# Optimization experiments

Measured on AMD Instinct MI355X. Metric: run time of the kernel, lower is better.

The kernel has to match this reference:

```python
import jax, jax.numpy as jnp
import numpy as np

N = 250000
E = 4000000
IN_F, HID, OUT = 18, 16, 1


def setup_inputs() -> dict:
    key = jax.random.key(0)
    ks = jax.random.split(key, 7)
    x = jax.random.normal(ks[0], (N, IN_F), dtype=jnp.float32)
    edge_index = jax.random.randint(ks[1], (2, E), 0, N, dtype=jnp.int64)
    # GCNConv params (PyG uses Glorot for weight, zeros for bias)
    W1 = jax.random.normal(ks[2], (IN_F, HID), dtype=jnp.float32) * (1.0 / np.sqrt(IN_F))
    b1 = jnp.zeros((HID,), dtype=jnp.float32)
    W2 = jax.random.normal(ks[3], (HID, OUT), dtype=jnp.float32) * (1.0 / np.sqrt(HID))
    b2 = jnp.zeros((OUT,), dtype=jnp.float32)
    return {"x": x, "edge_index": edge_index, "W1": W1, "b1": b1, "W2": W2, "b2": b2}


def _gcn_conv(x, W, b, src, dst, norm, n_nodes):
    # linear transform then degree-normalized scatter-add (PyG GCNConv)
    h = x @ W                                  # [N, F_out]
    msg = h[src] * norm[:, None]               # gather + per-edge scale
    out = jax.ops.segment_sum(msg, dst, num_segments=n_nodes)
    return out + b


def reference(x, edge_index, W1, b1, W2, b2):
    # add self-loops (GCNConv default add_self_loops=True)
    loops = jnp.arange(N, dtype=edge_index.dtype)
    src = jnp.concatenate([edge_index[0], loops])
    dst = jnp.concatenate([edge_index[1], loops])
    # symmetric normalization: deg computed at destination over self-looped graph
    deg = jax.ops.segment_sum(jnp.ones_like(dst, dtype=x.dtype), dst, num_segments=N)
    dis = jnp.where(deg > 0, jax.lax.rsqrt(deg), 0.0)
    norm = dis[src] * dis[dst]                 # [E+N]
    h = _gcn_conv(x, W1, b1, src, dst, norm, N)
    h = jax.nn.relu(h)
    # dropout is identity in eval mode (F.dropout(training=self.training))
    out = _gcn_conv(h, W2, b2, src, dst, norm, N)
    return out
```

## Files before the change

### kernel.cpp

```cpp
#include <hip/hip_runtime.h>
#include <hip/hip_fp16.h>


#define NB_BITS 8
#define BN (1 << NB_BITS)
#define SB_BITS 9
#define SBN (1 << SB_BITS)
#define NSB 512
#define BIN_TPB 512
#define BIN_CHUNK 8192
#define AGG_TPB 512

__device__ __forceinline__ int exscan512(int v, int* warpsums, int t) {
    int lane = t & 63, w = t >> 6;
    int x = v;
#pragma unroll
    for (int off = 1; off < 64; off <<= 1) {
        int y = __shfl_up(x, off);
        if (lane >= off) x += y;
    }
    if (lane == 63) warpsums[w] = x;
    __syncthreads();
    if (w == 0) {
        int s = (lane < 8) ? warpsums[lane] : 0;
#pragma unroll
        for (int off = 1; off < 8; off <<= 1) {
            int y = __shfl_up(s, off);
            if (lane >= off) s += y;
        }
        if (lane < 8) warpsums[lane] = s;
    }
    __syncthreads();
    int base = (w > 0) ? warpsums[w - 1] : 0;
    return base + x - v;
}

__global__ void bhist_kernel(const int* __restrict__ dst, int* __restrict__ bcnt, int E) {
    __shared__ int cnt[NSB];
    int t = threadIdx.x;
    cnt[t] = 0;
    __syncthreads();
    int base = blockIdx.x * BIN_CHUNK;
    int end = min(base + BIN_CHUNK, E);
    if (end - base == BIN_CHUNK) {
        const int4* d4 = (const int4*)(dst + base);
#pragma unroll
        for (int i = 0; i < BIN_CHUNK / (BIN_TPB * 4); i++) {
            int4 v = d4[t + i * BIN_TPB];
            atomicAdd(&cnt[v.x >> SB_BITS], 1);
            atomicAdd(&cnt[v.y >> SB_BITS], 1);
            atomicAdd(&cnt[v.z >> SB_BITS], 1);
            atomicAdd(&cnt[v.w >> SB_BITS], 1);
        }
    } else {
        for (int e = base + t; e < end; e += BIN_TPB)
            atomicAdd(&cnt[dst[e] >> SB_BITS], 1);
    }
    __syncthreads();
    if (cnt[t] > 0) atomicAdd(&bcnt[t], cnt[t]);
}

__global__ void bscan_kernel(const int* __restrict__ bcnt, int* __restrict__ bstart,
                             int* __restrict__ cursor) {
    __shared__ int warpsums[8];
    int t = threadIdx.x;
    int v = bcnt[t];
    int excl = exscan512(v, warpsums, t);
    bstart[t] = excl;
    cursor[t] = excl;
    if (t == NSB - 1) bstart[NSB] = excl + v;
}

__global__ void bplace_kernel(const int* __restrict__ src, const int* __restrict__ dst,
                              int* __restrict__ cursor, int* __restrict__ pairs, int E) {
    __shared__ int cnt[NSB];
    __shared__ int lstart[NSB];
    __shared__ int lcur[NSB];
    __shared__ int gbase[NSB];
    __shared__ int warpsums[8];
    __shared__ int lbuf[BIN_CHUNK];
    __shared__ unsigned short lbin[BIN_CHUNK];
    int t = threadIdx.x;
    int base = blockIdx.x * BIN_CHUNK;
    int end = min(base + BIN_CHUNK, E);
    int full = (end - base == BIN_CHUNK);
    cnt[t] = 0;
    __syncthreads();
    if (full) {
        const int4* d4 = (const int4*)(dst + base);
#pragma unroll
        for (int i = 0; i < BIN_CHUNK / (BIN_TPB * 4); i++) {
            int4 v = d4[t + i * BIN_TPB];
            atomicAdd(&cnt[v.x >> SB_BITS], 1);
            atomicAdd(&cnt[v.y >> SB_BITS], 1);
            atomicAdd(&cnt[v.z >> SB_BITS], 1);
            atomicAdd(&cnt[v.w >> SB_BITS], 1);
        }
    } else {
        for (int e = base + t; e < end; e += BIN_TPB)
            atomicAdd(&cnt[dst[e] >> SB_BITS], 1);
    }
    __syncthreads();
    int v = cnt[t];
    int excl = exscan512(v, warpsums, t);
    lstart[t] = excl;
    lcur[t] = excl;
    gbase[t] = (v > 0) ? atomicAdd(&cursor[t], v) : 0;
    __syncthreads();
    if (full) {
        const int4* s4 = (const int4*)(src + base);
        const int4* d4 = (const int4*)(dst + base);
#pragma unroll
        for (int i = 0; i < BIN_CHUNK / (BIN_TPB * 4); i++) {
            int4 dv = d4[t + i * BIN_TPB];
            int4 sv = s4[t + i * BIN_TPB];
            int b0 = dv.x >> SB_BITS, p0 = atomicAdd(&lcur[b0], 1);
            lbuf[p0] = (sv.x << SB_BITS) | (dv.x & (SBN - 1));
            lbin[p0] = (unsigned short)b0;
            int b1 = dv.y >> SB_BITS, p1 = atomicAdd(&lcur[b1], 1);
            lbuf[p1] = (sv.y << SB_BITS) | (dv.y & (SBN - 1));
            lbin[p1] = (unsigned short)b1;
            int b2 = dv.z >> SB_BITS, p2 = atomicAdd(&lcur[b2], 1);
            lbuf[p2] = (sv.z << SB_BITS) | (dv.z & (SBN - 1));
            lbin[p2] = (unsigned short)b2;
            int b3 = dv.w >> SB_BITS, p3 = atomicAdd(&lcur[b3], 1);
            lbuf[p3] = (sv.w << SB_BITS) | (dv.w & (SBN - 1));
            lbin[p3] = (unsigned short)b3;
        }
    } else {
        for (int e = base + t; e < end; e += BIN_TPB) {
            int d = dst[e], s = src[e];
            int b = d >> SB_BITS;
            int pos = atomicAdd(&lcur[b], 1);
            lbuf[pos] = (s << SB_BITS) | (d & (SBN - 1));
            lbin[pos] = (unsigned short)b;
        }
    }
    __syncthreads();
    int n = end - base;
#pragma unroll 4
    for (int i = t; i < n; i += BIN_TPB) {
        int b = lbin[i];
        pairs[gbase[b] + (i - lstart[b])] = lbuf[i];
    }
}

__global__ void csr_kernel(const int* __restrict__ pairs, const int* __restrict__ bstart,
                           int* __restrict__ rowp, int* __restrict__ csr_src,
                           float* __restrict__ dis, const float* __restrict__ x,
                           const float* __restrict__ W1, __half* __restrict__ hs1h,
                           int N) {
    __shared__ int cnt[SBN];
    __shared__ int warpsums[8];
    __shared__ float w[18 * 16];
    int b = blockIdx.x, t = threadIdx.x;
    int s0 = bstart[b], s1 = bstart[b + 1];
    cnt[t] = 0;
    if (t < 18 * 16) w[t] = W1[t];
    __syncthreads();
#pragma unroll 4
    for (int e = s0 + t; e < s1; e += SBN)
        atomicAdd(&cnt[pairs[e] & (SBN - 1)], 1);
    __syncthreads();
    int v = cnt[t];
    int excl = exscan512(v, warpsums, t);
    int nbase = b << SB_BITS;
    int start = s0 + excl;
    rowp[nbase + t] = start;
    int n = nbase + t;
    float dv = rsqrtf((float)v + 1.0f);
    if (n < N) dis[n] = dv;
    __syncthreads();
    cnt[t] = start;
    if (t == 0) rowp[nbase + SBN] = s1;
    __syncthreads();
#pragma unroll 4
    for (int e = s0 + t; e < s1; e += SBN) {
        int pv = pairs[e];
        int pos = atomicAdd(&cnt[pv & (SBN - 1)], 1);
        csr_src[pos] = pv >> SB_BITS;
    }
    if (n < N) {
        const float2* x2 = (const float2*)(x + (size_t)n * 18);
        float xv[18];
#pragma unroll
        for (int k = 0; k < 9; k++) {
            float2 vv = x2[k];
            xv[2 * k] = vv.x;
            xv[2 * k + 1] = vv.y;
        }
        float acc[16];
#pragma unroll
        for (int f = 0; f < 16; f++) acc[f] = 0.0f;
#pragma unroll
        for (int k = 0; k < 18; k++) {
            float xk = xv[k];
#pragma unroll
            for (int f = 0; f < 16; f++) acc[f] = fmaf(xk, w[k * 16 + f], acc[f]);
        }
        unsigned int u[8];
#pragma unroll
        for (int q = 0; q < 8; q++) {
            unsigned int lo = __half_as_ushort(__float2half_rn(acc[2 * q] * dv));
            unsigned int hi = __half_as_ushort(__float2half_rn(acc[2 * q + 1] * dv));
            u[q] = lo | (hi << 16);
        }
        uint4* outp = (uint4*)(hs1h + (size_t)n * 16);
        outp[0] = make_uint4(u[0], u[1], u[2], u[3]);
        outp[1] = make_uint4(u[4], u[5], u[6], u[7]);
    }
}

__global__ void agg1_kernel(const int* __restrict__ csr_src, const int* __restrict__ rowp,
                            const __half* __restrict__ hs1h, const float* __restrict__ dis,
                            const float* __restrict__ b1, const float* __restrict__ W2,
                            float* __restrict__ hs2, int N) {
    int b = blockIdx.x, t = threadIdx.x;
    int f = t & 15;
    int g = t >> 4;
    float bbf = b1[f], wwf = W2[f];
    int nbase = b << NB_BITS;
    for (int nl = g; nl < BN; nl += AGG_TPB / 16) {
        int n = nbase + nl;
        if (n >= N) continue;
        int r0 = rowp[n], r1 = rowp[n + 1];
        float a = 0.f;
#pragma unroll 4
        for (int r = r0; r < r1; ++r) {
            int s = csr_src[r];
            a += __half2float(hs1h[(size_t)s * 16 + f]);
        }
        float d = dis[n];
        float self = __half2float(hs1h[(size_t)n * 16 + f]);
        float p = fmaxf(d * (a + self) + bbf, 0.f) * wwf;
        p += __shfl_xor(p, 1);
        p += __shfl_xor(p, 2);
        p += __shfl_xor(p, 4);
        p += __shfl_xor(p, 8);
        if (f == 0) hs2[n] = p * d;
    }
}

__global__ void agg2_kernel(const int* __restrict__ csr_src, const int* __restrict__ rowp,
                            const float* __restrict__ hs2, const float* __restrict__ dis,
                            const float* __restrict__ b2, float* __restrict__ out, int N) {
    int b = blockIdx.x, t = threadIdx.x;
    int l = t & 15;
    int g = t >> 4;
    int nbase = b << NB_BITS;
    float bb = b2[0];
    for (int nl = g; nl < BN; nl += AGG_TPB / 16) {
        int n = nbase + nl;
        if (n >= N) continue;
        int r0 = rowp[n], r1 = rowp[n + 1];
        float a = 0.f;
        for (int r = r0 + l; r < r1; r += 16) a += hs2[csr_src[r]];
        a += __shfl_xor(a, 1);
        a += __shfl_xor(a, 2);
        a += __shfl_xor(a, 4);
        a += __shfl_xor(a, 8);
        if (l == 0) out[n] = dis[n] * (a + hs2[n]) + bb;
    }
}

extern "C" void kernel_launch(void* const* d_in, const int* in_sizes, int n_in,
                              void* d_out, int out_size, void* d_ws, size_t ws_size,
                              hipStream_t stream) {
    const float* x = (const float*)d_in[0];
    const int* edge_index = (const int*)d_in[1];
    const float* W1 = (const float*)d_in[2];
    const float* b1 = (const float*)d_in[3];
    const float* W2 = (const float*)d_in[4];
    const float* b2 = (const float*)d_in[5];
    float* out = (float*)d_out;

    const int N = in_sizes[0] / 18;
    const int E = in_sizes[1] / 2;
    const int* src = edge_index;
    const int* dst = edge_index + E;
    const int NABUCKET = (N + BN - 1) / BN;
    const int NSBUCKET = (N + SBN - 1) / SBN;

    int* ws = (int*)d_ws;
    int* pairs = ws;
    int* csr_src = pairs + (size_t)E;
    __half* hs1h = (__half*)(csr_src + (size_t)E);
    float* hs2 = (float*)((int*)(csr_src + (size_t)E) + 8 * (size_t)N);
    float* dis = hs2 + N;
    int* rowp = (int*)(dis + N);
    int* bstart = rowp + (size_t)NSBUCKET * SBN + 1;
    int* cursor = bstart + NSB + 1;
    int* bcnt = cursor + NSB;

    hipMemsetAsync(bcnt, 0, NSB * sizeof(int), stream);

    int binBlocks = (E + BIN_CHUNK - 1) / BIN_CHUNK;

    bhist_kernel<<<binBlocks, BIN_TPB, 0, stream>>>(dst, bcnt, E);
    bscan_kernel<<<1, NSB, 0, stream>>>(bcnt, bstart, cursor);
    bplace_kernel<<<binBlocks, BIN_TPB, 0, stream>>>(src, dst, cursor, pairs, E);
    csr_kernel<<<NSBUCKET, SBN, 0, stream>>>(pairs, bstart, rowp, csr_src, dis,
                                             x, W1, hs1h, N);
    agg1_kernel<<<NABUCKET, AGG_TPB, 0, stream>>>(csr_src, rowp, hs1h, dis, b1, W2, hs2, N);
    agg2_kernel<<<NABUCKET, AGG_TPB, 0, stream>>>(csr_src, rowp, hs2, dis, b2, out, N);
}
```

Baseline: 246.7 us.

## Replace global bucket histogram pass with per-chunk sort and segmented CSR build

Drops the global histogram and scan kernels. Each chunk now sorts its edges locally into buckets and writes them contiguously, along with per-chunk bucket offsets. The CSR kernel gathers its bucket's segments from every chunk and claims its output region with an atomic allocator, so rows no longer come out in global order and rowp gains a per-bucket layout. The dis array is removed and the normalisation is recomputed from the row length inside the aggregation kernels. This saves two launches and one full read of dst. The cost is that in the CSR kernel each thread walks one chunk's segment serially, giving uncoalesced, imbalanced loads with only about 489 of 512 threads active.

```diff
diff --git a/kernel.cpp b/kernel.cpp
--- a/kernel.cpp
+++ b/kernel.cpp
@@ -35,14 +35,19 @@
     return base + x - v;
 }
 
-__global__ void bhist_kernel(const int* __restrict__ dst, int* __restrict__ bcnt, int E) {
+__global__ void sortchunk_kernel(const int* __restrict__ src, const int* __restrict__ dst,
+                                 int* __restrict__ pairs, int* __restrict__ pofs, int E) {
     __shared__ int cnt[NSB];
-    int t = threadIdx.x;
+    __shared__ int lcur[NSB];
+    __shared__ int warpsums[8];
+    __shared__ int lbuf[BIN_CHUNK];
+    int t = threadIdx.x, c = blockIdx.x;
+    int base = c * BIN_CHUNK;
+    int end = min(base + BIN_CHUNK, E);
+    int full = (end - base == BIN_CHUNK);
     cnt[t] = 0;
     __syncthreads();
-    int base = blockIdx.x * BIN_CHUNK;
-    int end = min(base + BIN_CHUNK, E);
-    if (end - base == BIN_CHUNK) {
+    if (full) {
         const int4* d4 = (const int4*)(dst + base);
 #pragma unroll
         for (int i = 0; i < BIN_CHUNK / (BIN_TPB * 4); i++) {
@@ -57,55 +62,11 @@
             atomicAdd(&cnt[dst[e] >> SB_BITS], 1);
     }
     __syncthreads();
-    if (cnt[t] > 0) atomicAdd(&bcnt[t], cnt[t]);
-}
-
-__global__ void bscan_kernel(const int* __restrict__ bcnt, int* __restrict__ bstart,
-                             int* __restrict__ cursor) {
-    __shared__ int warpsums[8];
-    int t = threadIdx.x;
-    int v = bcnt[t];
-    int excl = exscan512(v, warpsums, t);
-    bstart[t] = excl;
-    cursor[t] = excl;
-    if (t == NSB - 1) bstart[NSB] = excl + v;
-}
-
-__global__ void bplace_kernel(const int* __restrict__ src, const int* __restrict__ dst,
-                              int* __restrict__ cursor, int* __restrict__ pairs, int E) {
-    __shared__ int cnt[NSB];
-    __shared__ int lstart[NSB];
-    __shared__ int lcur[NSB];
-    __shared__ int gbase[NSB];
-    __shared__ int warpsums[8];
-    __shared__ int lbuf[BIN_CHUNK];
-    __shared__ unsigned short lbin[BIN_CHUNK];
-    int t = threadIdx.x;
-    int base = blockIdx.x * BIN_CHUNK;
-    int end = min(base + BIN_CHUNK, E);
-    int full = (end - base == BIN_CHUNK);
-    cnt[t] = 0;
-    __syncthreads();
-    if (full) {
-        const int4* d4 = (const int4*)(dst + base);
-#pragma unroll
-        for (int i = 0; i < BIN_CHUNK / (BIN_TPB * 4); i++) {
-            int4 v = d4[t + i * BIN_TPB];
-            atomicAdd(&cnt[v.x >> SB_BITS], 1);
-            atomicAdd(&cnt[v.y >> SB_BITS], 1);
-            atomicAdd(&cnt[v.z >> SB_BITS], 1);
-            atomicAdd(&cnt[v.w >> SB_BITS], 1);
-        }
-    } else {
-        for (int e = base + t; e < end; e += BIN_TPB)
-            atomicAdd(&cnt[dst[e] >> SB_BITS], 1);
-    }
-    __syncthreads();
     int v = cnt[t];
     int excl = exscan512(v, warpsums, t);
-    lstart[t] = excl;
     lcur[t] = excl;
-    gbase[t] = (v > 0) ? atomicAdd(&cursor[t], v) : 0;
+    pofs[(size_t)c * (NSB + 1) + t] = excl;
+    if (t == 0) pofs[(size_t)c * (NSB + 1) + NSB] = end - base;
     __syncthreads();
     if (full) {
         const int4* s4 = (const int4*)(src + base);
@@ -116,16 +77,12 @@
             int4 sv = s4[t + i * BIN_TPB];
             int b0 = dv.x >> SB_BITS, p0 = atomicAdd(&lcur[b0], 1);
             lbuf[p0] = (sv.x << SB_BITS) | (dv.x & (SBN - 1));
-            lbin[p0] = (unsigned short)b0;
             int b1 = dv.y >> SB_BITS, p1 = atomicAdd(&lcur[b1], 1);
             lbuf[p1] = (sv.y << SB_BITS) | (dv.y & (SBN - 1));
-            lbin[p1] = (unsigned short)b1;
             int b2 = dv.z >> SB_BITS, p2 = atomicAdd(&lcur[b2], 1);
             lbuf[p2] = (sv.z << SB_BITS) | (dv.z & (SBN - 1));
-            lbin[p2] = (unsigned short)b2;
             int b3 = dv.w >> SB_BITS, p3 = atomicAdd(&lcur[b3], 1);
             lbuf[p3] = (sv.w << SB_BITS) | (dv.w & (SBN - 1));
-            lbin[p3] = (unsigned short)b3;
         }
     } else {
         for (int e = base + t; e < end; e += BIN_TPB) {
@@ -133,50 +90,52 @@
             int b = d >> SB_BITS;
             int pos = atomicAdd(&lcur[b], 1);
             lbuf[pos] = (s << SB_BITS) | (d & (SBN - 1));
-            lbin[pos] = (unsigned short)b;
         }
     }
     __syncthreads();
     int n = end - base;
 #pragma unroll 4
-    for (int i = t; i < n; i += BIN_TPB) {
-        int b = lbin[i];
-        pairs[gbase[b] + (i - lstart[b])] = lbuf[i];
-    }
-}
-
-__global__ void csr_kernel(const int* __restrict__ pairs, const int* __restrict__ bstart,
-                           int* __restrict__ rowp, int* __restrict__ csr_src,
-                           float* __restrict__ dis, const float* __restrict__ x,
+    for (int i = t; i < n; i += BIN_TPB) pairs[base + i] = lbuf[i];
+}
+
+__global__ void csr_kernel(const int* __restrict__ pairs, const int* __restrict__ pofs,
+                           int* __restrict__ alloc, int* __restrict__ rowp,
+                           int* __restrict__ csr_src, const float* __restrict__ x,
                            const float* __restrict__ W1, __half* __restrict__ hs1h,
-                           int N) {
+                           int N, int NCHUNK) {
     __shared__ int cnt[SBN];
     __shared__ int warpsums[8];
     __shared__ float w[18 * 16];
+    __shared__ int regbase_s;
     int b = blockIdx.x, t = threadIdx.x;
-    int s0 = bstart[b], s1 = bstart[b + 1];
     cnt[t] = 0;
     if (t < 18 * 16) w[t] = W1[t];
-    __syncthreads();
-#pragma unroll 4
-    for (int e = s0 + t; e < s1; e += SBN)
-        atomicAdd(&cnt[pairs[e] & (SBN - 1)], 1);
+    int seg0 = 0, seg1 = 0;
+    if (t < NCHUNK) {
+        int s = pofs[(size_t)t * (NSB + 1) + b];
+        int e = pofs[(size_t)t * (NSB + 1) + b + 1];
+        seg0 = t * BIN_CHUNK + s;
+        seg1 = t * BIN_CHUNK + e;
+    }
+    __syncthreads();
+    for (int i = seg0; i < seg1; ++i)
+        atomicAdd(&cnt[pairs[i] & (SBN - 1)], 1);
     __syncthreads();
     int v = cnt[t];
     int excl = exscan512(v, warpsums, t);
+    if (t == 0) regbase_s = atomicAdd(alloc, warpsums[7]);
+    __syncthreads();
+    int regbase = regbase_s;
     int nbase = b << SB_BITS;
-    int start = s0 + excl;
-    rowp[nbase + t] = start;
+    int start = regbase + excl;
+    rowp[(size_t)b * (SBN + 1) + t] = start;
+    if (t == 0) rowp[(size_t)b * (SBN + 1) + SBN] = regbase + warpsums[7];
     int n = nbase + t;
     float dv = rsqrtf((float)v + 1.0f);
-    if (n < N) dis[n] = dv;
-    __syncthreads();
     cnt[t] = start;
-    if (t == 0) rowp[nbase + SBN] = s1;
-    __syncthreads();
-#pragma unroll 4
-    for (int e = s0 + t; e < s1; e += SBN) {
-        int pv = pairs[e];
+    __syncthreads();
+    for (int i = seg0; i < seg1; ++i) {
+        int pv = pairs[i];
         int pos = atomicAdd(&cnt[pv & (SBN - 1)], 1);
         csr_src[pos] = pv >> SB_BITS;
     }
@@ -212,9 +171,8 @@
 }
 
 __global__ void agg1_kernel(const int* __restrict__ csr_src, const int* __restrict__ rowp,
-                            const __half* __restrict__ hs1h, const float* __restrict__ dis,
-                            const float* __restrict__ b1, const float* __restrict__ W2,
-                            float* __restrict__ hs2, int N) {
+                            const __half* __restrict__ hs1h, const float* __restrict__ b1,
+                            const float* __restrict__ W2, float* __restrict__ hs2, int N) {
     int b = blockIdx.x, t = threadIdx.x;
     int f = t & 15;
     int g = t >> 4;
@@ -223,14 +181,16 @@
     for (int nl = g; nl < BN; nl += AGG_TPB / 16) {
         int n = nbase + nl;
         if (n >= N) continue;
-        int r0 = rowp[n], r1 = rowp[n + 1];
+        int bb = n >> SB_BITS, ii = n & (SBN - 1);
+        int r0 = rowp[(size_t)bb * (SBN + 1) + ii];
+        int r1 = rowp[(size_t)bb * (SBN + 1) + ii + 1];
         float a = 0.f;
 #pragma unroll 4
         for (int r = r0; r < r1; ++r) {
             int s = csr_src[r];
             a += __half2float(hs1h[(size_t)s * 16 + f]);
         }
-        float d = dis[n];
+        float d = rsqrtf((float)(r1 - r0) + 1.0f);
         float self = __half2float(hs1h[(size_t)n * 16 + f]);
         float p = fmaxf(d * (a + self) + bbf, 0.f) * wwf;
         p += __shfl_xor(p, 1);
@@ -242,8 +202,8 @@
 }
 
 __global__ void agg2_kernel(const int* __restrict__ csr_src, const int* __restrict__ rowp,
-                            const float* __restrict__ hs2, const float* __restrict__ dis,
-                            const float* __restrict__ b2, float* __restrict__ out, int N) {
+                            const float* __restrict__ hs2, const float* __restrict__ b2,
+                            float* __restrict__ out, int N) {
     int b = blockIdx.x, t = threadIdx.x;
     int l = t & 15;
     int g = t >> 4;
@@ -252,14 +212,19 @@
     for (int nl = g; nl < BN; nl += AGG_TPB / 16) {
         int n = nbase + nl;
         if (n >= N) continue;
-        int r0 = rowp[n], r1 = rowp[n + 1];
+        int bbn = n >> SB_BITS, ii = n & (SBN - 1);
+        int r0 = rowp[(size_t)bbn * (SBN + 1) + ii];
+        int r1 = rowp[(size_t)bbn * (SBN + 1) + ii + 1];
         float a = 0.f;
         for (int r = r0 + l; r < r1; r += 16) a += hs2[csr_src[r]];
         a += __shfl_xor(a, 1);
         a += __shfl_xor(a, 2);
         a += __shfl_xor(a, 4);
         a += __shfl_xor(a, 8);
-        if (l == 0) out[n] = dis[n] * (a + hs2[n]) + bb;
+        if (l == 0) {
+            float d = rsqrtf((float)(r1 - r0) + 1.0f);
+            out[n] = d * (a + hs2[n]) + bb;
+        }
     }
 }
 
@@ -280,27 +245,22 @@
     const int* dst = edge_index + E;
     const int NABUCKET = (N + BN - 1) / BN;
     const int NSBUCKET = (N + SBN - 1) / SBN;
+    const int NCHUNK = (E + BIN_CHUNK - 1) / BIN_CHUNK;
 
     int* ws = (int*)d_ws;
     int* pairs = ws;
-    int* csr_src = pairs + (size_t)E;
+    int* csr_src = pairs + (size_t)NCHUNK * BIN_CHUNK;
     __half* hs1h = (__half*)(csr_src + (size_t)E);
     float* hs2 = (float*)((int*)(csr_src + (size_t)E) + 8 * (size_t)N);
-    float* dis = hs2 + N;
-    int* rowp = (int*)(dis + N);
-    int* bstart = rowp + (size_t)NSBUCKET * SBN + 1;
-    int* cursor = bstart + NSB + 1;
-    int* bcnt = cursor + NSB;
-
-    hipMemsetAsync(bcnt, 0, NSB * sizeof(int), stream);
-
-    int binBlocks = (E + BIN_CHUNK - 1) / BIN_CHUNK;
-
-    bhist_kernel<<<binBlocks, BIN_TPB, 0, stream>>>(dst, bcnt, E);
-    bscan_kernel<<<1, NSB, 0, stream>>>(bcnt, bstart, cursor);
-    bplace_kernel<<<binBlocks, BIN_TPB, 0, stream>>>(src, dst, cursor, pairs, E);
-    csr_kernel<<<NSBUCKET, SBN, 0, stream>>>(pairs, bstart, rowp, csr_src, dis,
-                                             x, W1, hs1h, N);
-    agg1_kernel<<<NABUCKET, AGG_TPB, 0, stream>>>(csr_src, rowp, hs1h, dis, b1, W2, hs2, N);
-    agg2_kernel<<<NABUCKET, AGG_TPB, 0, stream>>>(csr_src, rowp, hs2, dis, b2, out, N);
-}
+    int* rowp = (int*)(hs2 + N);
+    int* pofs = rowp + (size_t)NSBUCKET * (SBN + 1);
+    int* alloc = pofs + (size_t)NCHUNK * (NSB + 1);
+
+    hipMemsetAsync(alloc, 0, sizeof(int), stream);
+
+    sortchunk_kernel<<<NCHUNK, BIN_TPB, 0, stream>>>(src, dst, pairs, pofs, E);
+    csr_kernel<<<NSBUCKET, SBN, 0, stream>>>(pairs, pofs, alloc, rowp, csr_src,
+                                             x, W1, hs1h, N, NCHUNK);
+    agg1_kernel<<<NABUCKET, AGG_TPB, 0, stream>>>(csr_src, rowp, hs1h, b1, W2, hs2, N);
+    agg2_kernel<<<NABUCKET, AGG_TPB, 0, stream>>>(csr_src, rowp, hs2, b2, out, N);
+}
```

After: 289.4 us. 17.3% more time.
